# Performance work log

Hardware: AMD Instinct MI355X
Metric: run time of the kernel (lower is better)

Reference implementation:

```python
import jax, jax.numpy as jnp
import numpy as np

NUM_FEATURES = 256
NUM_HEADS = 8
HEAD_SIZE = NUM_FEATURES // NUM_HEADS  # 32
N_AGENTS = 8
B = 32
SEQ = 64


def setup_inputs() -> dict:
    key = jax.random.key(0)
    ks = jax.random.split(key, 6)
    s = 0.02
    x = jax.random.normal(ks[0], (N_AGENTS * B, NUM_FEATURES, SEQ), dtype=jnp.float32)
    Wq = jax.random.normal(ks[1], (NUM_HEADS, NUM_FEATURES, HEAD_SIZE), dtype=jnp.float32) * s
    Wk = jax.random.normal(ks[2], (NUM_HEADS, NUM_FEATURES, HEAD_SIZE), dtype=jnp.float32) * s
    Wv = jax.random.normal(ks[3], (NUM_HEADS, NUM_FEATURES, HEAD_SIZE), dtype=jnp.float32) * s
    Wp = jax.random.normal(ks[4], (NUM_FEATURES, NUM_FEATURES), dtype=jnp.float32) * s
    bp = jnp.zeros((NUM_FEATURES,), dtype=jnp.float32)
    return {"x": x, "Wq": Wq, "Wk": Wk, "Wv": Wv, "Wp": Wp, "bp": bp, "n_agents": N_AGENTS}


def reference(x, Wq, Wk, Wv, Wp, bp, n_agents):
    # x: (n_agents*b, f, h)
    b_total, f, h = x.shape
    b = b_total // n_agents
    # reshape + rearrange 'n b f h -> n b h f'  (t = token axis of length h)
    xs = x.reshape(n_agents, b, f, h).transpose(0, 1, 3, 2)  # (n, b, t, f)
    # All heads at once: per-head linear projections (no bias)
    q = jnp.einsum('nbtf,Hfd->Hnbtd', xs, Wq)
    k = jnp.einsum('nbtf,Hfd->Hnbtd', xs, Wk)
    v = jnp.einsum('nbtf,Hfd->Hnbtd', xs, Wv)
    # all-pairs agent attention: i = key agent, j = query agent
    scale = f ** (-0.5)  # source scales by num_features, not head_size
    scores = jnp.einsum('Hjbtd,Hibsd->Hijbts', q, k) * scale  # (H,n,n,b,t,s)
    attn = jax.nn.softmax(scores, axis=-1)
    # weighted values, then sum over key-agent axis i
    out = jnp.einsum('Hijbts,Hibsd->Hjbtd', attn, v)  # (H,n,b,t,d)
    # concat heads on last dim (head 0 first), matching torch.cat
    y = jnp.moveaxis(out, 0, 3).reshape(n_agents, b, h, f)  # (n,b,t,H*d)
    # output projection (dropout is identity at eval / p=0)
    y = jnp.einsum('nbtf,gf->nbtg', y, Wp) + bp
    # rearrange 'n b h f -> n b f h' then merge agents into batch
    y = y.transpose(0, 1, 3, 2).reshape(n_agents * b, f, h)
    return y
```

## Files before the change

### kernel.cpp

```cpp
#include <hip/hip_runtime.h>

#define F   256
#define T   64
#define NH  8
#define D   32
#define NA  8
#define NBB 32

typedef unsigned short ushortT;
typedef unsigned int   uintT;

typedef short bf16x8 __attribute__((ext_vector_type(8)));
typedef float f32x4  __attribute__((ext_vector_type(4)));

__device__ __forceinline__ float bf2f(ushortT u) {
    union { uintT i; float f; } c; c.i = ((uintT)u) << 16; return c.f;
}
__device__ __forceinline__ ushortT f2bf(float f) {
    union { float f; uintT u; } c; c.f = f;
    uintT u = c.u;
    uintT r = u + 0x7fffu + ((u >> 16) & 1u);
    return (ushortT)(r >> 16);
}

__device__ __forceinline__ uintT cvt_pk_bf16(float lo, float hi) {
    uintT r;
    asm("v_cvt_pk_bf16_f32 %0, %1, %2" : "=v"(r) : "v"(lo), "v"(hi));
    return r;
}
__device__ __forceinline__ void packc1(const f32x4 v, uintT& u0, uintT& u1) {
    u0 = cvt_pk_bf16(v[0], v[1]);
    u1 = cvt_pk_bf16(v[2], v[3]);
}
__device__ __forceinline__ void packcs(const f32x4 v, float s, uintT& u0, uintT& u1) {
    u0 = cvt_pk_bf16(v[0] * s, v[1] * s);
    u1 = cvt_pk_bf16(v[2] * s, v[3] * s);
}

__device__ __forceinline__ float fexp2(float x) {
#if __has_builtin(__builtin_amdgcn_exp2f)
    return __builtin_amdgcn_exp2f(x);
#else
    float r; asm("v_exp_f32 %0, %1" : "=v"(r) : "v"(x)); return r;
#endif
}
__device__ __forceinline__ float frcp(float x) {
#if __has_builtin(__builtin_amdgcn_rcpf)
    return __builtin_amdgcn_rcpf(x);
#else
    float r; asm("v_rcp_f32 %0, %1" : "=v"(r) : "v"(x)); return r;
#endif
}

__device__ __forceinline__ int detect_isbf16(const void* xraw) {
    const uintT* w = (const uintT*)xraw;
    int bad = 0;
    for (int k = 0; k < 128; ++k) {
        uintT v = w[k];
        uintT e0 = (v >> 7)  & 0xffu;
        uintT e1 = (v >> 23) & 0xffu;
        bad += (e0 > 131u) + (e1 > 131u);
    }
    return bad == 0 ? 1 : 0;
}

__device__ __forceinline__ ushortT cvt_elem(const void* p, size_t i, bool isbf) {
    return isbf ? ((const ushortT*)p)[i] : f2bf(((const float*)p)[i]);
}

__device__ __forceinline__ bf16x8 build_frag(uintT u0a, uintT u1a, uintT u0b, uintT u1b,
                                             int sl0, int sl1, bool hi) {
    union { uintT u[4]; bf16x8 v; } r;
    uintT x0a = (uintT)__shfl((int)u0a, sl0), x0b = (uintT)__shfl((int)u0b, sl0);
    uintT x1a = (uintT)__shfl((int)u1a, sl0), x1b = (uintT)__shfl((int)u1b, sl0);
    uintT x2a = (uintT)__shfl((int)u0a, sl1), x2b = (uintT)__shfl((int)u0b, sl1);
    uintT x3a = (uintT)__shfl((int)u1a, sl1), x3b = (uintT)__shfl((int)u1b, sl1);
    r.u[0] = hi ? x0b : x0a;
    r.u[1] = hi ? x1b : x1a;
    r.u[2] = hi ? x2b : x2a;
    r.u[3] = hi ? x3b : x3a;
    return r.v;
}

__device__ __forceinline__ int xposU(int t, int f) {
    return t * 256 + ((((f >> 3) ^ (t & 31)) * 8) | (f & 7));
}
#define FRAGPOS(t_, ks_, quad_) \
    ((t_) * 256 + ((((4 * (ks_) + (quad_)) ^ ((t_) & 31)) * 8)))


__global__ __launch_bounds__(256) void wprep_kernel(const void* __restrict__ Wq,
                                                    const void* __restrict__ Wk,
                                                    const void* __restrict__ Wv,
                                                    const void* __restrict__ Wp,
                                                    const void* __restrict__ x,
                                                    ushortT* __restrict__ Wt) {
    __shared__ int sflag;
    if (threadIdx.x == 0) sflag = detect_isbf16(x);
    __syncthreads();
    bool isbf = sflag != 0;

    int base = (blockIdx.x * 256 + threadIdx.x) * 8;
    int cp = base >> 8, f0 = base & 255;

    ushortT tmp[8];
    if (cp < 768) {
        int qkv = cp >> 8, c = cp & 255, hh = c >> 5, d = c & 31;
        const void* W = (qkv == 0) ? Wq : (qkv == 1) ? Wk : Wv;
        #pragma unroll
        for (int jj = 0; jj < 8; ++jj)
            tmp[jj] = cvt_elem(W, (size_t)(hh * F + f0 + jj) * D + d, isbf);
    } else {
        int g = cp - 768;
        #pragma unroll
        for (int jj = 0; jj < 8; ++jj)
            tmp[jj] = cvt_elem(Wp, (size_t)g * F + f0 + jj, isbf);
    }
    *(uint4*)&Wt[base] = *(const uint4*)tmp;
}

template <int NT>
__device__ __forceinline__ void stage_xT(const void* x, int nb, ushortT* xs,
                                         bool isbf, int tid) {
    int t = tid & 63;
    int g0 = tid >> 6;
    const int GP = NT / 64;
    #pragma unroll
    for (int it = 0; it < 64 / GP; ++it) {
        int g = g0 + it * GP;
        float v0, v1, v2, v3;
        if (isbf) {
            const ushortT* xp = (const ushortT*)x + (size_t)nb * (F * T) + (size_t)g * 4 * T + t;
            v0 = bf2f(xp[0]); v1 = bf2f(xp[T]); v2 = bf2f(xp[2 * T]); v3 = bf2f(xp[3 * T]);
        } else {
            const float* xp = (const float*)x + (size_t)nb * (F * T) + (size_t)g * 4 * T + t;
            v0 = xp[0]; v1 = xp[T]; v2 = xp[2 * T]; v3 = xp[3 * T];
        }
        uintT lo  = cvt_pk_bf16(v0, v1);
        uintT hi2 = cvt_pk_bf16(v2, v3);
        *(uint2*)&xs[xposU(t & 31, g * 4) + (t >> 5) * 8192] = make_uint2(lo, hi2);
    }
}

__global__ __launch_bounds__(256) void qkv_kernel(const void* __restrict__ x,
                                                  const ushortT* __restrict__ Wt,
                                                  ushortT* __restrict__ Kws,
                                                  ushortT* __restrict__ Vws) {
    int nb = blockIdx.x, half = blockIdx.y;
    __shared__ __align__(16) ushortT xs[T * F];
    __shared__ int sflag;
    int tid = threadIdx.x;
    if (tid == 0) sflag = detect_isbf16(x);
    __syncthreads();
    bool isbf = sflag != 0;
    stage_xT<256>(x, nb, xs, isbf, tid);
    __syncthreads();

    int w = tid >> 6, lane = tid & 63, l15 = lane & 15, quad = lane >> 4;
    int rowbase = 256 + 256 * half + 64 * w;

    f32x4 acc[4][4];
    #pragma unroll
    for (int a = 0; a < 4; ++a)
        #pragma unroll
        for (int c = 0; c < 4; ++c) acc[a][c] = (f32x4){0.f, 0.f, 0.f, 0.f};

    #pragma unroll
    for (int ks = 0; ks < 8; ++ks) {
        bf16x8 Bfr[4];
        #pragma unroll
        for (int nt = 0; nt < 4; ++nt) {
            int t = 16 * nt + l15;
            Bfr[nt] = *(const bf16x8*)&xs[FRAGPOS(t & 31, ks, quad) + (t >> 5) * 8192];
        }
        #pragma unroll
        for (int mt = 0; mt < 4; ++mt) {
            bf16x8 Afr = *(const bf16x8*)(Wt +
                (size_t)(rowbase + 16 * mt + l15) * 256 + ks * 32 + quad * 8);
            #pragma unroll
            for (int nt = 0; nt < 4; ++nt)
                acc[mt][nt] = __builtin_amdgcn_mfma_f32_16x16x32_bf16(Afr, Bfr[nt],
                                                                      acc[mt][nt], 0, 0, 0);
        }
    }

    #pragma unroll
    for (int mt = 0; mt < 4; ++mt) {
        int rel = 64 * w + 16 * mt + 4 * quad;
        int hh = rel >> 5, db = rel & 31;
        #pragma unroll
        for (int nt = 0; nt < 4; ++nt) {
            int t = 16 * nt + l15;
            f32x4 v = acc[mt][nt];
            if (half == 0) {
                ushortT* dst = Kws + ((size_t)(nb * NH + hh) * T + t) * D + db;
                uintT lo  = cvt_pk_bf16(v[0], v[1]);
                uintT hi2 = cvt_pk_bf16(v[2], v[3]);
                *(uint2*)dst = make_uint2(lo, hi2);
            } else {
                uintT p0 = cvt_pk_bf16(v[0], v[1]);
                uintT p1 = cvt_pk_bf16(v[2], v[3]);
                size_t vb = (size_t)(nb * NH + hh) * D + db;
                Vws[(vb + 0) * T + t] = (ushortT)p0;
                Vws[(vb + 1) * T + t] = (ushortT)(p0 >> 16);
                Vws[(vb + 2) * T + t] = (ushortT)p1;
                Vws[(vb + 3) * T + t] = (ushortT)(p1 >> 16);
            }
        }
    }
}

__global__ __launch_bounds__(512, 2) void attn_kernel(const void* __restrict__ x,
                                                      const ushortT* __restrict__ Wt,
                                                      const ushortT* __restrict__ Kws,
                                                      const ushortT* __restrict__ Vws,
                                                      const void* __restrict__ bp,
                                                      void* __restrict__ outp) {
    __shared__ __align__(16) ushortT xs[32 * F];
    __shared__ float bpf[F];
    __shared__ int sflag;

    int tid = threadIdx.x;
    int b = blockIdx.x, j = blockIdx.y, tb = blockIdx.z;
    int nbj = j * NBB + b;

    if (tid == 0) sflag = detect_isbf16(x);
    __syncthreads();
    bool isbf = sflag != 0;

    {
        int t = tid & 31, fg = tid >> 5;
        int ta = tb * 32 + t;
        #pragma unroll
        for (int it = 0; it < 4; ++it) {
            int f0 = (fg + 16 * it) * 4;
            float v0, v1, v2, v3;
            if (isbf) {
                const ushortT* xp = (const ushortT*)x + (size_t)nbj * (F * T) +
                                    (size_t)f0 * T + ta;
                v0 = bf2f(xp[0]); v1 = bf2f(xp[T]); v2 = bf2f(xp[2 * T]); v3 = bf2f(xp[3 * T]);
            } else {
                const float* xp = (const float*)x + (size_t)nbj * (F * T) +
                                  (size_t)f0 * T + ta;
                v0 = xp[0]; v1 = xp[T]; v2 = xp[2 * T]; v3 = xp[3 * T];
            }
            uintT lo  = cvt_pk_bf16(v0, v1);
            uintT hi2 = cvt_pk_bf16(v2, v3);
            *(uint2*)&xs[xposU(t, f0)] = make_uint2(lo, hi2);
        }
    }
    if (tid < 256)
        bpf[tid] = isbf ? bf2f(((const ushortT*)bp)[tid]) : ((const float*)bp)[tid];
    __syncthreads();

    int h = tid >> 6, lane = tid & 63, l15 = lane & 15, quad = lane >> 4;
    bool hi = quad >= 2;
    int sl0 = l15 + 32 * (quad & 1), sl1 = sl0 + 16;

    const float QS = 0.0625f * 1.44269504089f;
    bf16x8 qf[2];
    {
        f32x4 qacc[2][2];
        #pragma unroll
        for (int mt = 0; mt < 2; ++mt)
            #pragma unroll
            for (int nt = 0; nt < 2; ++nt) qacc[mt][nt] = (f32x4){0.f, 0.f, 0.f, 0.f};
        #pragma unroll
        for (int ks = 0; ks < 8; ++ks) {
            bf16x8 xf[2];
            #pragma unroll
            for (int nt = 0; nt < 2; ++nt)
                xf[nt] = *(const bf16x8*)&xs[FRAGPOS(16 * nt + l15, ks, quad)];
            #pragma unroll
            for (int mt = 0; mt < 2; ++mt) {
                bf16x8 Aw = *(const bf16x8*)(Wt +
                    (size_t)(32 * h + 16 * mt + l15) * 256 + ks * 32 + quad * 8);
                #pragma unroll
                for (int nt = 0; nt < 2; ++nt)
                    qacc[mt][nt] = __builtin_amdgcn_mfma_f32_16x16x32_bf16(
                        Aw, xf[nt], qacc[mt][nt], 0, 0, 0);
            }
        }
        #pragma unroll
        for (int tt = 0; tt < 2; ++tt) {
            uintT a0, a1, b0, b1;
            packcs(qacc[0][tt], QS, a0, a1);
            packcs(qacc[1][tt], QS, b0, b1);
            qf[tt] = build_frag(a0, a1, b0, b1, sl0, sl1, hi);
        }
    }

    f32x4 oacc[2][2];
    #pragma unroll
    for (int mt = 0; mt < 2; ++mt)
        #pragma unroll
        for (int tt = 0; tt < 2; ++tt) oacc[mt][tt] = (f32x4){0.f, 0.f, 0.f, 0.f};

    for (int i = 0; i < NA; ++i) {
        int nbi = i * NBB + b;
        const ushortT* Kb = Kws + (size_t)(nbi * NH + h) * T * D;
        const ushortT* Vb = Vws + (size_t)(nbi * NH + h) * D * T;

        float psum[2] = {0.f, 0.f};
        f32x4 pv[2][2];
        #pragma unroll
        for (int mt = 0; mt < 2; ++mt)
            #pragma unroll
            for (int tt = 0; tt < 2; ++tt) pv[mt][tt] = (f32x4){0.f, 0.f, 0.f, 0.f};

        #pragma unroll
        for (int kx = 0; kx < 2; ++kx) {
            bf16x8 kfr[2];
            kfr[0] = *(const bf16x8*)(Kb + (16 * (2 * kx + 0) + l15) * D + quad * 8);
            kfr[1] = *(const bf16x8*)(Kb + (16 * (2 * kx + 1) + l15) * D + quad * 8);
            bf16x8 vf0 = *(const bf16x8*)(Vb + l15 * T + kx * 32 + quad * 8);
            bf16x8 vf1 = *(const bf16x8*)(Vb + (16 + l15) * T + kx * 32 + quad * 8);

            uintT pu0[2][2], pu1[2][2];
            #pragma unroll
            for (int sp = 0; sp < 2; ++sp) {
                #pragma unroll
                for (int tt = 0; tt < 2; ++tt) {
                    f32x4 s4 = __builtin_amdgcn_mfma_f32_16x16x32_bf16(
                        kfr[sp], qf[tt], (f32x4){0.f, 0.f, 0.f, 0.f}, 0, 0, 0);
                    float e0 = fexp2(s4[0]);
                    float e1 = fexp2(s4[1]);
                    float e2 = fexp2(s4[2]);
                    float e3 = fexp2(s4[3]);
                    psum[tt] += (e0 + e1) + (e2 + e3);
                    pu0[sp][tt] = cvt_pk_bf16(e0, e1);
                    pu1[sp][tt] = cvt_pk_bf16(e2, e3);
                }
            }
            #pragma unroll
            for (int tt = 0; tt < 2; ++tt) {
                bf16x8 pf = build_frag(pu0[0][tt], pu1[0][tt], pu0[1][tt], pu1[1][tt],
                                       sl0, sl1, hi);
                pv[0][tt] = __builtin_amdgcn_mfma_f32_16x16x32_bf16(
                    vf0, pf, pv[0][tt], 0, 0, 0);
                pv[1][tt] = __builtin_amdgcn_mfma_f32_16x16x32_bf16(
                    vf1, pf, pv[1][tt], 0, 0, 0);
            }
        }

        #pragma unroll
        for (int tt = 0; tt < 2; ++tt) {
            float s = psum[tt];
            s += __shfl_xor(s, 16);
            s += __shfl_xor(s, 32);
            float inv = frcp(s);
            #pragma unroll
            for (int mt = 0; mt < 2; ++mt)
                #pragma unroll
                for (int r = 0; r < 4; ++r)
                    oacc[mt][tt][r] = fmaf(inv, pv[mt][tt][r], oacc[mt][tt][r]);
        }
    }

    __syncthreads();
    #pragma unroll
    for (int mt = 0; mt < 2; ++mt)
        #pragma unroll
        for (int tt = 0; tt < 2; ++tt) {
            int t = 16 * tt + l15;
            int cb = 32 * h + 16 * mt + 4 * quad;
            uintT u0, u1;
            packc1(oacc[mt][tt], u0, u1);
            *(uint2*)&xs[xposU(t, cb)] = make_uint2(u0, u1);
        }
    __syncthreads();

    f32x4 cacc[2][2];
    #pragma unroll
    for (int a = 0; a < 2; ++a)
        #pragma unroll
        for (int c = 0; c < 2; ++c) cacc[a][c] = (f32x4){0.f, 0.f, 0.f, 0.f};

    #pragma unroll
    for (int ks = 0; ks < 8; ++ks) {
        bf16x8 yb[2];
        #pragma unroll
        for (int nt = 0; nt < 2; ++nt)
            yb[nt] = *(const bf16x8*)&xs[FRAGPOS(16 * nt + l15, ks, quad)];
        #pragma unroll
        for (int m2 = 0; m2 < 2; ++m2) {
            int g = 16 * (2 * h + m2) + l15;
            bf16x8 wf = *(const bf16x8*)(Wt + (size_t)(768 + g) * 256 + ks * 32 + quad * 8);
            #pragma unroll
            for (int nt = 0; nt < 2; ++nt)
                cacc[m2][nt] = __builtin_amdgcn_mfma_f32_16x16x32_bf16(
                    wf, yb[nt], cacc[m2][nt], 0, 0, 0);
        }
    }

    #pragma unroll
    for (int m2 = 0; m2 < 2; ++m2)
        #pragma unroll
        for (int nt = 0; nt < 2; ++nt) {
            int t = tb * 32 + 16 * nt + l15;
            #pragma unroll
            for (int r = 0; r < 4; ++r) {
                int g = 16 * (2 * h + m2) + 4 * quad + r;
                float val = cacc[m2][nt][r] + bpf[g];
                if (isbf)
                    ((ushortT*)outp)[(size_t)nbj * F * T + g * T + t] = f2bf(val);
                else
                    ((float*)outp)[(size_t)nbj * F * T + g * T + t] = val;
            }
        }
}

__device__ __forceinline__ float tof(ushortT u) { return bf2f(u); }
__device__ __forceinline__ float tof(float f)   { return f; }

__device__ __forceinline__ void stage_x(const void* x, size_t nb, ushortT* sX,
                                        bool isbf, int tid) {
    if (isbf) {
        const int4* xg = (const int4*)((const ushortT*)x + nb * (F * T));
        int4* xl = (int4*)sX;
        for (int kk = tid; kk < F * T / 8; kk += 512) xl[kk] = xg[kk];
    } else {
        const float4* xg = (const float4*)((const float*)x + nb * (F * T));
        for (int kk = tid; kk < F * T / 4; kk += 512) {
            float4 v = xg[kk];
            int o = kk * 4;
            sX[o + 0] = f2bf(v.x); sX[o + 1] = f2bf(v.y);
            sX[o + 2] = f2bf(v.z); sX[o + 3] = f2bf(v.w);
        }
    }
}

template <typename WT>
__device__ __forceinline__ void q_proj(const WT* __restrict__ W, const ushortT* sX,
                                       ushortT* dst, int c, int t0) {
    float acc[32];
    #pragma unroll
    for (int m = 0; m < 32; ++m) acc[m] = 0.f;
    for (int f = 0; f < F; ++f) {
        float w = tof(W[f * D]);
        const ushortT* xr = &sX[f * T + t0];
        #pragma unroll
        for (int m = 0; m < 32; ++m) acc[m] = fmaf(bf2f(xr[m]), w, acc[m]);
    }
    #pragma unroll
    for (int m = 0; m < 32; ++m) dst[(t0 + m) * F + c] = f2bf(acc[m]);
}

template <typename WT>
__device__ __forceinline__ void kv_proj(const WT* __restrict__ WK, const WT* __restrict__ WV,
                                        const ushortT* sX, ushortT* sK, ushortT* sV,
                                        int c, int t0) {
    float ak[32], av[32];
    #pragma unroll
    for (int m = 0; m < 32; ++m) { ak[m] = 0.f; av[m] = 0.f; }
    for (int f = 0; f < F; ++f) {
        float wk = tof(WK[f * D]);
        float wv = tof(WV[f * D]);
        const ushortT* xr = &sX[f * T + t0];
        #pragma unroll
        for (int m = 0; m < 32; ++m) {
            float xv = bf2f(xr[m]);
            ak[m] = fmaf(xv, wk, ak[m]);
            av[m] = fmaf(xv, wv, av[m]);
        }
    }
    #pragma unroll
    for (int m = 0; m < 32; ++m) {
        sK[(t0 + m) * F + c] = f2bf(ak[m]);
        sV[(t0 + m) * F + c] = f2bf(av[m]);
    }
}

__global__ __launch_bounds__(512) void fused_kernel(const void* __restrict__ x,
                                                    const void* __restrict__ Wq,
                                                    const void* __restrict__ Wk,
                                                    const void* __restrict__ Wv,
                                                    const void* __restrict__ Wp,
                                                    const void* __restrict__ bp,
                                                    void* __restrict__ outp) {
    __shared__ __align__(16) char smem[98304];
    __shared__ int sflag;
    ushortT* sX = (ushortT*)smem;
    ushortT* sK = (ushortT*)(smem + 32768);
    ushortT* sV = (ushortT*)(smem + 65536);
    float*   sO = (float*)smem;

    int tid = threadIdx.x;
    int b = blockIdx.x, j = blockIdx.y;
    size_t nbj = (size_t)j * NBB + b;

    if (tid == 0) sflag = detect_isbf16(x);
    __syncthreads();
    bool isbf = sflag != 0;

    stage_x(x, nbj, sX, isbf, tid);
    __syncthreads();

    int c = tid & 255, t0 = (tid >> 8) * 32;
    int hc = c >> 5, dc = c & 31;
    if (isbf) q_proj((const ushortT*)Wq + (size_t)hc * F * D + dc, sX, sK, c, t0);
    else      q_proj((const float*)Wq   + (size_t)hc * F * D + dc, sX, sK, c, t0);
    __syncthreads();

    int h = tid >> 6, t = tid & 63;
    float q[32], o[32];
    #pragma unroll
    for (int dd = 0; dd < 32; ++dd) { q[dd] = bf2f(sK[t * F + h * D + dd]); o[dd] = 0.f; }

    for (int i = 0; i < NA; ++i) {
        __syncthreads();
        stage_x(x, (size_t)(i * NBB + b), sX, isbf, tid);
        __syncthreads();
        if (isbf) kv_proj((const ushortT*)Wk + (size_t)hc * F * D + dc,
                          (const ushortT*)Wv + (size_t)hc * F * D + dc, sX, sK, sV, c, t0);
        else      kv_proj((const float*)Wk   + (size_t)hc * F * D + dc,
                          (const float*)Wv   + (size_t)hc * F * D + dc, sX, sK, sV, c, t0);
        __syncthreads();
        float l = 0.f;
        float oi[32];
        #pragma unroll
        for (int dd = 0; dd < 32; ++dd) oi[dd] = 0.f;
        for (int s = 0; s < T; ++s) {
            const ushortT* kr = &sK[s * F + h * D];
            float dot = 0.f;
            #pragma unroll
            for (int dd = 0; dd < 32; ++dd) dot = fmaf(q[dd], bf2f(kr[dd]), dot);
            float e = __expf(dot * 0.0625f);
            l += e;
            const ushortT* vr = &sV[s * F + h * D];
            #pragma unroll
            for (int dd = 0; dd < 32; ++dd) oi[dd] = fmaf(e, bf2f(vr[dd]), oi[dd]);
        }
        float inv = 1.0f / l;
        #pragma unroll
        for (int dd = 0; dd < 32; ++dd) o[dd] = fmaf(inv, oi[dd], o[dd]);
    }
    __syncthreads();

    #pragma unroll
    for (int dd = 0; dd < 32; ++dd) sO[(h * D + dd) * T + t] = o[dd];
    __syncthreads();

    {
        int g = tid >> 1, te0 = (tid & 1) * 32;
        float acc[32];
        #pragma unroll
        for (int m = 0; m < 32; ++m) acc[m] = 0.f;
        if (isbf) {
            const ushortT* Wrow = (const ushortT*)Wp + (size_t)g * F;
            for (int cc = 0; cc < F; ++cc) {
                float w = bf2f(Wrow[cc]);
                const float* yr = &sO[cc * T + te0];
                #pragma unroll
                for (int m = 0; m < 32; ++m) acc[m] = fmaf(yr[m], w, acc[m]);
            }
        } else {
            const float* Wrow = (const float*)Wp + (size_t)g * F;
            for (int cc = 0; cc < F; ++cc) {
                float w = Wrow[cc];
                const float* yr = &sO[cc * T + te0];
                #pragma unroll
                for (int m = 0; m < 32; ++m) acc[m] = fmaf(yr[m], w, acc[m]);
            }
        }
        float bias = isbf ? bf2f(((const ushortT*)bp)[g]) : ((const float*)bp)[g];
        if (isbf) {
            ushortT* ob = (ushortT*)outp + nbj * F * T + g * T + te0;
            #pragma unroll
            for (int m = 0; m < 32; ++m) ob[m] = f2bf(acc[m] + bias);
        } else {
            float* ob = (float*)outp + nbj * F * T + g * T + te0;
            #pragma unroll
            for (int m = 0; m < 32; ++m) ob[m] = acc[m] + bias;
        }
    }
}

extern "C" void kernel_launch(void* const* d_in, const int* in_sizes, int n_in,
                              void* d_out, int out_size, void* d_ws, size_t ws_size,
                              hipStream_t stream) {
    const void* x  = d_in[0];
    const void* Wq = d_in[1];
    const void* Wk = d_in[2];
    const void* Wv = d_in[3];
    const void* Wp = d_in[4];
    const void* bp = d_in[5];

    const size_t needA = 17301504;

    if (ws_size >= needA) {
        char* ws = (char*)d_ws;
        ushortT* Wt  = (ushortT*)(ws + 0);
        ushortT* Kws = (ushortT*)(ws + 524288);
        ushortT* Vws = (ushortT*)(ws + 8912896);

        wprep_kernel<<<dim3(128),      dim3(256), 0, stream>>>(Wq, Wk, Wv, Wp, x, Wt);
        qkv_kernel  <<<dim3(256, 2),   dim3(256), 0, stream>>>(x, Wt, Kws, Vws);
        attn_kernel <<<dim3(32, 8, 2), dim3(512), 0, stream>>>(x, Wt, Kws, Vws, bp, d_out);
    } else {
        fused_kernel<<<dim3(32, 8), dim3(512), 0, stream>>>(x, Wq, Wk, Wv, Wp, bp, d_out);
    }
}
```

Before: 148.7 us.

## Split token axis finer in qkv and attention kernels for more blocks

The qkv kernel now splits the 64 tokens into two 32-token halves across a new grid dimension, and the attention kernel processes 16 query tokens per block instead of 32, doubling both grids. Shared memory per block shrinks and per-thread accumulators halve, so occupancy and parallelism on the many CUs can rise. In exchange, each attention block reloads the full K/V for all agents and the Wp/Wq weights for half as much work, and x staging is repeated, increasing redundant global and L2 traffic.

```diff
diff --git a/kernel.cpp b/kernel.cpp
--- a/kernel.cpp
+++ b/kernel.cpp
@@ -119,66 +119,62 @@
     *(uint4*)&Wt[base] = *(const uint4*)tmp;
 }
 
-template <int NT>
-__device__ __forceinline__ void stage_xT(const void* x, int nb, ushortT* xs,
-                                         bool isbf, int tid) {
-    int t = tid & 63;
-    int g0 = tid >> 6;
-    const int GP = NT / 64;
-    #pragma unroll
-    for (int it = 0; it < 64 / GP; ++it) {
-        int g = g0 + it * GP;
-        float v0, v1, v2, v3;
-        if (isbf) {
-            const ushortT* xp = (const ushortT*)x + (size_t)nb * (F * T) + (size_t)g * 4 * T + t;
-            v0 = bf2f(xp[0]); v1 = bf2f(xp[T]); v2 = bf2f(xp[2 * T]); v3 = bf2f(xp[3 * T]);
-        } else {
-            const float* xp = (const float*)x + (size_t)nb * (F * T) + (size_t)g * 4 * T + t;
-            v0 = xp[0]; v1 = xp[T]; v2 = xp[2 * T]; v3 = xp[3 * T];
-        }
-        uintT lo  = cvt_pk_bf16(v0, v1);
-        uintT hi2 = cvt_pk_bf16(v2, v3);
-        *(uint2*)&xs[xposU(t & 31, g * 4) + (t >> 5) * 8192] = make_uint2(lo, hi2);
-    }
-}
-
 __global__ __launch_bounds__(256) void qkv_kernel(const void* __restrict__ x,
                                                   const ushortT* __restrict__ Wt,
                                                   ushortT* __restrict__ Kws,
                                                   ushortT* __restrict__ Vws) {
-    int nb = blockIdx.x, half = blockIdx.y;
-    __shared__ __align__(16) ushortT xs[T * F];
+    int nb = blockIdx.x, half = blockIdx.y, th = blockIdx.z;
+    __shared__ __align__(16) ushortT xs[32 * F];
     __shared__ int sflag;
     int tid = threadIdx.x;
     if (tid == 0) sflag = detect_isbf16(x);
     __syncthreads();
     bool isbf = sflag != 0;
-    stage_xT<256>(x, nb, xs, isbf, tid);
+
+    {
+        int t = tid & 31, g0 = tid >> 5;
+        int ta = th * 32 + t;
+        #pragma unroll
+        for (int it = 0; it < 8; ++it) {
+            int g = g0 + 8 * it;
+            float v0, v1, v2, v3;
+            if (isbf) {
+                const ushortT* xp = (const ushortT*)x + (size_t)nb * (F * T) +
+                                    (size_t)g * 4 * T + ta;
+                v0 = bf2f(xp[0]); v1 = bf2f(xp[T]); v2 = bf2f(xp[2 * T]); v3 = bf2f(xp[3 * T]);
+            } else {
+                const float* xp = (const float*)x + (size_t)nb * (F * T) +
+                                  (size_t)g * 4 * T + ta;
+                v0 = xp[0]; v1 = xp[T]; v2 = xp[2 * T]; v3 = xp[3 * T];
+            }
+            uintT lo  = cvt_pk_bf16(v0, v1);
+            uintT hi2 = cvt_pk_bf16(v2, v3);
+            *(uint2*)&xs[xposU(t, g * 4)] = make_uint2(lo, hi2);
+        }
+    }
     __syncthreads();
 
     int w = tid >> 6, lane = tid & 63, l15 = lane & 15, quad = lane >> 4;
     int rowbase = 256 + 256 * half + 64 * w;
 
-    f32x4 acc[4][4];
+    f32x4 acc[4][2];
     #pragma unroll
     for (int a = 0; a < 4; ++a)
         #pragma unroll
-        for (int c = 0; c < 4; ++c) acc[a][c] = (f32x4){0.f, 0.f, 0.f, 0.f};
+        for (int c = 0; c < 2; ++c) acc[a][c] = (f32x4){0.f, 0.f, 0.f, 0.f};
 
     #pragma unroll
     for (int ks = 0; ks < 8; ++ks) {
-        bf16x8 Bfr[4];
-        #pragma unroll
-        for (int nt = 0; nt < 4; ++nt) {
-            int t = 16 * nt + l15;
-            Bfr[nt] = *(const bf16x8*)&xs[FRAGPOS(t & 31, ks, quad) + (t >> 5) * 8192];
-        }
+        bf16x8 Bfr[2];
+        #pragma unroll
+        for (int nt = 0; nt < 2; ++nt)
+            Bfr[nt] = *(const bf16x8*)&xs[FRAGPOS(16 * nt + l15, ks, quad)];
         #pragma unroll
         for (int mt = 0; mt < 4; ++mt) {
             bf16x8 Afr = *(const bf16x8*)(Wt +
                 (size_t)(rowbase + 16 * mt + l15) * 256 + ks * 32 + quad * 8);
             #pragma unroll
-            for (int nt = 0; nt < 4; ++nt)
+            for (int nt = 0; nt < 2; ++nt)
                 acc[mt][nt] = __builtin_amdgcn_mfma_f32_16x16x32_bf16(Afr, Bfr[nt],
                                                                       acc[mt][nt], 0, 0, 0);
         }
@@ -189,8 +185,8 @@
         int rel = 64 * w + 16 * mt + 4 * quad;
         int hh = rel >> 5, db = rel & 31;
         #pragma unroll
-        for (int nt = 0; nt < 4; ++nt) {
-            int t = 16 * nt + l15;
+        for (int nt = 0; nt < 2; ++nt) {
+            int t = th * 32 + 16 * nt + l15;
             f32x4 v = acc[mt][nt];
             if (half == 0) {
                 ushortT* dst = Kws + ((size_t)(nb * NH + hh) * T + t) * D + db;
@@ -210,13 +206,13 @@
     }
 }
 
-__global__ __launch_bounds__(512, 2) void attn_kernel(const void* __restrict__ x,
-                                                      const ushortT* __restrict__ Wt,
-                                                      const ushortT* __restrict__ Kws,
-                                                      const ushortT* __restrict__ Vws,
-                                                      const void* __restrict__ bp,
-                                                      void* __restrict__ outp) {
-    __shared__ __align__(16) ushortT xs[32 * F];
+__global__ __launch_bounds__(512) void attn_kernel(const void* __restrict__ x,
+                                                   const ushortT* __restrict__ Wt,
+                                                   const ushortT* __restrict__ Kws,
+                                                   const ushortT* __restrict__ Vws,
+                                                   const void* __restrict__ bp,
+                                                   void* __restrict__ outp) {
+    __shared__ __align__(16) ushortT xs[16 * F];
     __shared__ float bpf[F];
     __shared__ int sflag;
 
@@ -229,11 +225,11 @@
     bool isbf = sflag != 0;
 
     {
-        int t = tid & 31, fg = tid >> 5;
-        int ta = tb * 32 + t;
-        #pragma unroll
-        for (int it = 0; it < 4; ++it) {
-            int f0 = (fg + 16 * it) * 4;
+        int t = tid & 15, fg = tid >> 4;
+        int ta = tb * 16 + t;
+        #pragma unroll
+        for (int it = 0; it < 2; ++it) {
+            int f0 = (fg + 32 * it) * 4;
             float v0, v1, v2, v3;
             if (isbf) {
                 const ushortT* xp = (const ushortT*)x + (size_t)nbj * (F * T) +
@@ -258,55 +254,41 @@
     int sl0 = l15 + 32 * (quad & 1), sl1 = sl0 + 16;
 
     const float QS = 0.0625f * 1.44269504089f;
-    bf16x8 qf[2];
+    bf16x8 qf;
     {
-        f32x4 qacc[2][2];
-        #pragma unroll
-        for (int mt = 0; mt < 2; ++mt)
-            #pragma unroll
-            for (int nt = 0; nt < 2; ++nt) qacc[mt][nt] = (f32x4){0.f, 0.f, 0.f, 0.f};
+        f32x4 qacc[2];
+        qacc[0] = (f32x4){0.f, 0.f, 0.f, 0.f};
+        qacc[1] = (f32x4){0.f, 0.f, 0.f, 0.f};
         #pragma unroll
         for (int ks = 0; ks < 8; ++ks) {
-            bf16x8 xf[2];
-            #pragma unroll
-            for (int nt = 0; nt < 2; ++nt)
-                xf[nt] = *(const bf16x8*)&xs[FRAGPOS(16 * nt + l15, ks, quad)];
+            bf16x8 xf = *(const bf16x8*)&xs[FRAGPOS(l15, ks, quad)];
             #pragma unroll
             for (int mt = 0; mt < 2; ++mt) {
                 bf16x8 Aw = *(const bf16x8*)(Wt +
                     (size_t)(32 * h + 16 * mt + l15) * 256 + ks * 32 + quad * 8);
-                #pragma unroll
-                for (int nt = 0; nt < 2; ++nt)
-                    qacc[mt][nt] = __builtin_amdgcn_mfma_f32_16x16x32_bf16(
-                        Aw, xf[nt], qacc[mt][nt], 0, 0, 0);
-            }
-        }
-        #pragma unroll
-        for (int tt = 0; tt < 2; ++tt) {
-            uintT a0, a1, b0, b1;
-            packcs(qacc[0][tt], QS, a0, a1);
-            packcs(qacc[1][tt], QS, b0, b1);
-            qf[tt] = build_frag(a0, a1, b0, b1, sl0, sl1, hi);
-        }
-    }
-
-    f32x4 oacc[2][2];
-    #pragma unroll
-    for (int mt = 0; mt < 2; ++mt)
-        #pragma unroll
-        for (int tt = 0; tt < 2; ++tt) oacc[mt][tt] = (f32x4){0.f, 0.f, 0.f, 0.f};
+                qacc[mt] = __builtin_amdgcn_mfma_f32_16x16x32_bf16(
+                    Aw, xf, qacc[mt], 0, 0, 0);
+            }
+        }
+        uintT a0, a1, b0, b1;
+        packcs(qacc[0], QS, a0, a1);
+        packcs(qacc[1], QS, b0, b1);
+        qf = build_frag(a0, a1, b0, b1, sl0, sl1, hi);
+    }
+
+    f32x4 oacc[2];
+    oacc[0] = (f32x4){0.f, 0.f, 0.f, 0.f};
+    oacc[1] = (f32x4){0.f, 0.f, 0.f, 0.f};
 
     for (int i = 0; i < NA; ++i) {
         int nbi = i * NBB + b;
         const ushortT* Kb = Kws + (size_t)(nbi * NH + h) * T * D;
         const ushortT* Vb = Vws + (size_t)(nbi * NH + h) * D * T;
 
-        float psum[2] = {0.f, 0.f};
-        f32x4 pv[2][2];
-        #pragma unroll
-        for (int mt = 0; mt < 2; ++mt)
-            #pragma unroll
-            for (int tt = 0; tt < 2; ++tt) pv[mt][tt] = (f32x4){0.f, 0.f, 0.f, 0.f};
+        float psum = 0.f;
+        f32x4 pv[2];
+        pv[0] = (f32x4){0.f, 0.f, 0.f, 0.f};
+        pv[1] = (f32x4){0.f, 0.f, 0.f, 0.f};
 
         #pragma unroll
         for (int kx = 0; kx < 2; ++kx) {
@@ -316,98 +298,75 @@
             bf16x8 vf0 = *(const bf16x8*)(Vb + l15 * T + kx * 32 + quad * 8);
             bf16x8 vf1 = *(const bf16x8*)(Vb + (16 + l15) * T + kx * 32 + quad * 8);
 
-            uintT pu0[2][2], pu1[2][2];
+            uintT pu0[2], pu1[2];
             #pragma unroll
             for (int sp = 0; sp < 2; ++sp) {
-                #pragma unroll
-                for (int tt = 0; tt < 2; ++tt) {
-                    f32x4 s4 = __builtin_amdgcn_mfma_f32_16x16x32_bf16(
-                        kfr[sp], qf[tt], (f32x4){0.f, 0.f, 0.f, 0.f}, 0, 0, 0);
-                    float e0 = fexp2(s4[0]);
-                    float e1 = fexp2(s4[1]);
-                    float e2 = fexp2(s4[2]);
-                    float e3 = fexp2(s4[3]);
-                    psum[tt] += (e0 + e1) + (e2 + e3);
-                    pu0[sp][tt] = cvt_pk_bf16(e0, e1);
-                    pu1[sp][tt] = cvt_pk_bf16(e2, e3);
-                }
-            }
-            #pragma unroll
-            for (int tt = 0; tt < 2; ++tt) {
-                bf16x8 pf = build_frag(pu0[0][tt], pu1[0][tt], pu0[1][tt], pu1[1][tt],
-                                       sl0, sl1, hi);
-                pv[0][tt] = __builtin_amdgcn_mfma_f32_16x16x32_bf16(
-                    vf0, pf, pv[0][tt], 0, 0, 0);
-                pv[1][tt] = __builtin_amdgcn_mfma_f32_16x16x32_bf16(
-                    vf1, pf, pv[1][tt], 0, 0, 0);
-            }
-        }
-
-        #pragma unroll
-        for (int tt = 0; tt < 2; ++tt) {
-            float s = psum[tt];
-            s += __shfl_xor(s, 16);
-            s += __shfl_xor(s, 32);
-            float inv = frcp(s);
-            #pragma unroll
-            for (int mt = 0; mt < 2; ++mt)
-                #pragma unroll
-                for (int r = 0; r < 4; ++r)
-                    oacc[mt][tt][r] = fmaf(inv, pv[mt][tt][r], oacc[mt][tt][r]);
-        }
-    }
-
-    __syncthreads();
-    #pragma unroll
-    for (int mt = 0; mt < 2; ++mt)
-        #pragma unroll
-        for (int tt = 0; tt < 2; ++tt) {
-            int t = 16 * tt + l15;
-            int cb = 32 * h + 16 * mt + 4 * quad;
-            uintT u0, u1;
-            packc1(oacc[mt][tt], u0, u1);
-            *(uint2*)&xs[xposU(t, cb)] = make_uint2(u0, u1);
-        }
-    __syncthreads();
-
-    f32x4 cacc[2][2];
-    #pragma unroll
-    for (int a = 0; a < 2; ++a)
-        #pragma unroll
-        for (int c = 0; c < 2; ++c) cacc[a][c] = (f32x4){0.f, 0.f, 0.f, 0.f};
+                f32x4 s4 = __builtin_amdgcn_mfma_f32_16x16x32_bf16(
+                    kfr[sp], qf, (f32x4){0.f, 0.f, 0.f, 0.f}, 0, 0, 0);
+                float e0 = fexp2(s4[0]);
+                float e1 = fexp2(s4[1]);
+                float e2 = fexp2(s4[2]);
+                float e3 = fexp2(s4[3]);
+                psum += (e0 + e1) + (e2 + e3);
+                pu0[sp] = cvt_pk_bf16(e0, e1);
+                pu1[sp] = cvt_pk_bf16(e2, e3);
+            }
+            bf16x8 pf = build_frag(pu0[0], pu1[0], pu0[1], pu1[1], sl0, sl1, hi);
+            pv[0] = __builtin_amdgcn_mfma_f32_16x16x32_bf16(vf0, pf, pv[0], 0, 0, 0);
+            pv[1] = __builtin_amdgcn_mfma_f32_16x16x32_bf16(vf1, pf, pv[1], 0, 0, 0);
+        }
+
+        float s = psum;
+        s += __shfl_xor(s, 16);
+        s += __shfl_xor(s, 32);
+        float inv = frcp(s);
+        #pragma unroll
+        for (int mt = 0; mt < 2; ++mt)
+            #pragma unroll
+            for (int r = 0; r < 4; ++r)
+                oacc[mt][r] = fmaf(inv, pv[mt][r], oacc[mt][r]);
+    }
+
+    __syncthreads();
+    #pragma unroll
+    for (int mt = 0; mt < 2; ++mt) {
+        int t = l15;
+        int cb = 32 * h + 16 * mt + 4 * quad;
+        uintT u0, u1;
+        packc1(oacc[mt], u0, u1);
+        *(uint2*)&xs[xposU(t, cb)] = make_uint2(u0, u1);
+    }
+    __syncthreads();
+
+    f32x4 cacc[2];
+    cacc[0] = (f32x4){0.f, 0.f, 0.f, 0.f};
+    cacc[1] = (f32x4){0.f, 0.f, 0.f, 0.f};
 
     #pragma unroll
     for (int ks = 0; ks < 8; ++ks) {
-        bf16x8 yb[2];
-        #pragma unroll
-        for (int nt = 0; nt < 2; ++nt)
-            yb[nt] = *(const bf16x8*)&xs[FRAGPOS(16 * nt + l15, ks, quad)];
+        bf16x8 yb = *(const bf16x8*)&xs[FRAGPOS(l15, ks, quad)];
         #pragma unroll
         for (int m2 = 0; m2 < 2; ++m2) {
             int g = 16 * (2 * h + m2) + l15;
             bf16x8 wf = *(const bf16x8*)(Wt + (size_t)(768 + g) * 256 + ks * 32 + quad * 8);
-            #pragma unroll
-            for (int nt = 0; nt < 2; ++nt)
-                cacc[m2][nt] = __builtin_amdgcn_mfma_f32_16x16x32_bf16(
-                    wf, yb[nt], cacc[m2][nt], 0, 0, 0);
-        }
-    }
-
-    #pragma unroll
-    for (int m2 = 0; m2 < 2; ++m2)
-        #pragma unroll
-        for (int nt = 0; nt < 2; ++nt) {
-            int t = tb * 32 + 16 * nt + l15;
-            #pragma unroll
-            for (int r = 0; r < 4; ++r) {
-                int g = 16 * (2 * h + m2) + 4 * quad + r;
-                float val = cacc[m2][nt][r] + bpf[g];
-                if (isbf)
-                    ((ushortT*)outp)[(size_t)nbj * F * T + g * T + t] = f2bf(val);
-                else
-                    ((float*)outp)[(size_t)nbj * F * T + g * T + t] = val;
-            }
-        }
+            cacc[m2] = __builtin_amdgcn_mfma_f32_16x16x32_bf16(
+                wf, yb, cacc[m2], 0, 0, 0);
+        }
+    }
+
+    #pragma unroll
+    for (int m2 = 0; m2 < 2; ++m2) {
+        int t = tb * 16 + l15;
+        #pragma unroll
+        for (int r = 0; r < 4; ++r) {
+            int g = 16 * (2 * h + m2) + 4 * quad + r;
+            float val = cacc[m2][r] + bpf[g];
+            if (isbf)
+                ((ushortT*)outp)[(size_t)nbj * F * T + g * T + t] = f2bf(val);
+            else
+                ((float*)outp)[(size_t)nbj * F * T + g * T + t] = val;
+        }
+    }
 }
 
 __device__ __forceinline__ float tof(ushortT u) { return bf2f(u); }
@@ -594,9 +553,9 @@
         ushortT* Kws = (ushortT*)(ws + 524288);
         ushortT* Vws = (ushortT*)(ws + 8912896);
 
-        wprep_kernel<<<dim3(128),      dim3(256), 0, stream>>>(Wq, Wk, Wv, Wp, x, Wt);
-        qkv_kernel  <<<dim3(256, 2),   dim3(256), 0, stream>>>(x, Wt, Kws, Vws);
-        attn_kernel <<<dim3(32, 8, 2), dim3(512), 0, stream>>>(x, Wt, Kws, Vws, bp, d_out);
+        wprep_kernel<<<dim3(128),         dim3(256), 0, stream>>>(Wq, Wk, Wv, Wp, x, Wt);
+        qkv_kernel  <<<dim3(256, 2, 2),   dim3(256), 0, stream>>>(x, Wt, Kws, Vws);
+        attn_kernel <<<dim3(32, 8, 4),    dim3(512), 0, stream>>>(x, Wt, Kws, Vws, bp, d_out);
     } else {
         fused_kernel<<<dim3(32, 8), dim3(512), 0, stream>>>(x, Wq, Wk, Wv, Wp, bp, d_out);
     }
```

Result: slower. 186.8 us (+25.6%).

## Double-buffer K tiles into LDS via async global_load_lds in attention loop

Applied to the files above, without the earlier changes.

The attention kernel now prefetches the next agent's K tile directly into a per-wave double-buffered LDS region with global_load_lds, and hoists all V fragment loads to the top of each iteration, waiting with an explicit vmcnt. This is meant to hide global-memory latency for K/V behind the MFMA and exp work of the current agent. LDS use grows by 64 KB per block and the second launch-bounds occupancy hint is dropped, which can reduce occupancy. The bias staging in LDS and the flag broadcast are also removed in favour of direct per-thread loads.

```diff
diff --git a/kernel.cpp b/kernel.cpp
--- a/kernel.cpp
+++ b/kernel.cpp
@@ -87,6 +87,18 @@
 }
 #define FRAGPOS(t_, ks_, quad_) \
     ((t_) * 256 + ((((4 * (ks_) + (quad_)) ^ ((t_) & 31)) * 8)))
+
+__device__ __forceinline__ void stage_K(const ushortT* Kb, ushortT* dst,
+                                        int l15, int quad) {
+    #pragma unroll
+    for (int c = 0; c < 4; ++c) {
+        const ushortT* g = Kb + (16 * c + l15) * D + quad * 8;
+        __builtin_amdgcn_global_load_lds(
+            (const __attribute__((address_space(1))) uintT*)g,
+            (__attribute__((address_space(3))) uintT*)(dst + c * 512),
+            16, 0, 0);
+    }
+}
 
 
 __global__ __launch_bounds__(256) void wprep_kernel(const void* __restrict__ Wq,
@@ -210,23 +222,20 @@
     }
 }
 
-__global__ __launch_bounds__(512, 2) void attn_kernel(const void* __restrict__ x,
-                                                      const ushortT* __restrict__ Wt,
-                                                      const ushortT* __restrict__ Kws,
-                                                      const ushortT* __restrict__ Vws,
-                                                      const void* __restrict__ bp,
-                                                      void* __restrict__ outp) {
+__global__ __launch_bounds__(512) void attn_kernel(const void* __restrict__ x,
+                                                   const ushortT* __restrict__ Wt,
+                                                   const ushortT* __restrict__ Kws,
+                                                   const ushortT* __restrict__ Vws,
+                                                   const void* __restrict__ bp,
+                                                   void* __restrict__ outp) {
+    __shared__ __align__(16) ushortT kbuf[NH * 4096];
     __shared__ __align__(16) ushortT xs[32 * F];
-    __shared__ float bpf[F];
-    __shared__ int sflag;
 
     int tid = threadIdx.x;
     int b = blockIdx.x, j = blockIdx.y, tb = blockIdx.z;
     int nbj = j * NBB + b;
 
-    if (tid == 0) sflag = detect_isbf16(x);
-    __syncthreads();
-    bool isbf = sflag != 0;
+    bool isbf = detect_isbf16(x) != 0;
 
     {
         int t = tid & 31, fg = tid >> 5;
@@ -249,13 +258,17 @@
             *(uint2*)&xs[xposU(t, f0)] = make_uint2(lo, hi2);
         }
     }
-    if (tid < 256)
-        bpf[tid] = isbf ? bf2f(((const ushortT*)bp)[tid]) : ((const float*)bp)[tid];
     __syncthreads();
 
     int h = tid >> 6, lane = tid & 63, l15 = lane & 15, quad = lane >> 4;
     bool hi = quad >= 2;
     int sl0 = l15 + 32 * (quad & 1), sl1 = sl0 + 16;
+
+    ushortT* kw = kbuf + h * 4096;
+    const size_t AG = (size_t)NBB * NH * T * D;
+    const ushortT* Kb0 = Kws + ((size_t)b * NH + h) * T * D;
+
+    stage_K(Kb0, kw, l15, quad);
 
     const float QS = 0.0625f * 1.44269504089f;
     bf16x8 qf[2];
@@ -297,9 +310,19 @@
         for (int tt = 0; tt < 2; ++tt) oacc[mt][tt] = (f32x4){0.f, 0.f, 0.f, 0.f};
 
     for (int i = 0; i < NA; ++i) {
-        int nbi = i * NBB + b;
-        const ushortT* Kb = Kws + (size_t)(nbi * NH + h) * T * D;
-        const ushortT* Vb = Vws + (size_t)(nbi * NH + h) * D * T;
+        const ushortT* Kbn = Kb0 + (size_t)((i < 7) ? i + 1 : 0) * AG;
+        stage_K(Kbn, kw + (((i & 1) ^ 1) << 11), l15, quad);
+
+        const ushortT* Vb = Vws + ((size_t)((i * NBB + b) * NH) + h) * D * T;
+        bf16x8 vf00 = *(const bf16x8*)(Vb + l15 * T + quad * 8);
+        bf16x8 vf01 = *(const bf16x8*)(Vb + (16 + l15) * T + quad * 8);
+        bf16x8 vf10 = *(const bf16x8*)(Vb + l15 * T + 32 + quad * 8);
+        bf16x8 vf11 = *(const bf16x8*)(Vb + (16 + l15) * T + 32 + quad * 8);
+
+        asm volatile("s_waitcnt vmcnt(8)" ::: "memory");
+        __builtin_amdgcn_sched_barrier(0);
+
+        const ushortT* kcur = kw + ((i & 1) << 11);
 
         float psum[2] = {0.f, 0.f};
         f32x4 pv[2][2];
@@ -310,19 +333,14 @@
 
         #pragma unroll
         for (int kx = 0; kx < 2; ++kx) {
-            bf16x8 kfr[2];
-            kfr[0] = *(const bf16x8*)(Kb + (16 * (2 * kx + 0) + l15) * D + quad * 8);
-            kfr[1] = *(const bf16x8*)(Kb + (16 * (2 * kx + 1) + l15) * D + quad * 8);
-            bf16x8 vf0 = *(const bf16x8*)(Vb + l15 * T + kx * 32 + quad * 8);
-            bf16x8 vf1 = *(const bf16x8*)(Vb + (16 + l15) * T + kx * 32 + quad * 8);
-
             uintT pu0[2][2], pu1[2][2];
             #pragma unroll
             for (int sp = 0; sp < 2; ++sp) {
+                bf16x8 kf = *(const bf16x8*)&kcur[(2 * kx + sp) * 512 + lane * 8];
                 #pragma unroll
                 for (int tt = 0; tt < 2; ++tt) {
                     f32x4 s4 = __builtin_amdgcn_mfma_f32_16x16x32_bf16(
-                        kfr[sp], qf[tt], (f32x4){0.f, 0.f, 0.f, 0.f}, 0, 0, 0);
+                        kf, qf[tt], (f32x4){0.f, 0.f, 0.f, 0.f}, 0, 0, 0);
                     float e0 = fexp2(s4[0]);
                     float e1 = fexp2(s4[1]);
                     float e2 = fexp2(s4[2]);
@@ -332,14 +350,16 @@
                     pu1[sp][tt] = cvt_pk_bf16(e2, e3);
                 }
             }
+            bf16x8 va  = kx ? vf10 : vf00;
+            bf16x8 vb2 = kx ? vf11 : vf01;
             #pragma unroll
             for (int tt = 0; tt < 2; ++tt) {
                 bf16x8 pf = build_frag(pu0[0][tt], pu1[0][tt], pu0[1][tt], pu1[1][tt],
                                        sl0, sl1, hi);
                 pv[0][tt] = __builtin_amdgcn_mfma_f32_16x16x32_bf16(
-                    vf0, pf, pv[0][tt], 0, 0, 0);
+                    va, pf, pv[0][tt], 0, 0, 0);
                 pv[1][tt] = __builtin_amdgcn_mfma_f32_16x16x32_bf16(
-                    vf1, pf, pv[1][tt], 0, 0, 0);
+                    vb2, pf, pv[1][tt], 0, 0, 0);
             }
         }
 
@@ -401,7 +421,9 @@
             #pragma unroll
             for (int r = 0; r < 4; ++r) {
                 int g = 16 * (2 * h + m2) + 4 * quad + r;
-                float val = cacc[m2][nt][r] + bpf[g];
+                float bpv = isbf ? bf2f(((const ushortT*)bp)[g])
+                                 : ((const float*)bp)[g];
+                float val = cacc[m2][nt][r] + bpv;
                 if (isbf)
                     ((ushortT*)outp)[(size_t)nbj * F * T + g * T + t] = f2bf(val);
                 else
@@ -594,9 +616,9 @@
         ushortT* Kws = (ushortT*)(ws + 524288);
         ushortT* Vws = (ushortT*)(ws + 8912896);
 
-        wprep_kernel<<<dim3(128),      dim3(256), 0, stream>>>(Wq, Wk, Wv, Wp, x, Wt);
-        qkv_kernel  <<<dim3(256, 2),   dim3(256), 0, stream>>>(x, Wt, Kws, Vws);
-        attn_kernel <<<dim3(32, 8, 2), dim3(512), 0, stream>>>(x, Wt, Kws, Vws, bp, d_out);
+        wprep_kernel<<<dim3(128),       dim3(256), 0, stream>>>(Wq, Wk, Wv, Wp, x, Wt);
+        qkv_kernel  <<<dim3(256, 2),    dim3(256), 0, stream>>>(x, Wt, Kws, Vws);
+        attn_kernel <<<dim3(32, 8, 2),  dim3(512), 0, stream>>>(x, Wt, Kws, Vws, bp, d_out);
     } else {
         fused_kernel<<<dim3(32, 8), dim3(512), 0, stream>>>(x, Wq, Wk, Wv, Wp, bp, d_out);
     }
```

Result: slower. 152.6 us (+2.6%).
